# Kernel optimization log

Measured on AMD Instinct MI355X. Metric: run time of the kernel, lower is better.

Reference implementation:

```python
import jax, jax.numpy as jnp
import numpy as np
import math

HIDDEN, HEADS, D_K = 768, 12, 64
BS, SEQ = 4, 2048


def setup_inputs() -> dict:
    key = jax.random.key(0)
    ks = jax.random.split(key, 5)
    s = 1.0 / math.sqrt(HIDDEN)
    return {
        "x": jax.random.normal(ks[0], (BS, SEQ, HIDDEN), dtype=jnp.float32),
        "Wq": jax.random.normal(ks[1], (HIDDEN, HIDDEN), dtype=jnp.float32) * s,
        "bq": jnp.zeros((HIDDEN,), jnp.float32),
        "Wk": jax.random.normal(ks[2], (HIDDEN, HIDDEN), dtype=jnp.float32) * s,
        "bk": jnp.zeros((HIDDEN,), jnp.float32),
        "Wv": jax.random.normal(ks[3], (HIDDEN, HIDDEN), dtype=jnp.float32) * s,
        "bv": jnp.zeros((HIDDEN,), jnp.float32),
        "Wo": jax.random.normal(ks[4], (HIDDEN, HIDDEN), dtype=jnp.float32) * s,
        "bo": jnp.zeros((HIDDEN,), jnp.float32),
    }


def reference(x, Wq, bq, Wk, bk, Wv, bv, Wo, bo):
    bs, seq, _ = x.shape
    # projections; nn.Linear computes x @ W.T + b
    def proj(W, b):
        y = jnp.einsum("bsd,ed->bse", x, W) + b
        return y.reshape(bs, seq, HEADS, D_K).transpose(0, 2, 1, 3)  # [b,h,s,d]
    q, k, v = proj(Wq, bq), proj(Wk, bk), proj(Wv, bv)
    scores = jnp.einsum("bhqd,bhkd->bhqk", q, k) / jnp.sqrt(jnp.float32(D_K))
    attn = jax.nn.softmax(scores, axis=-1)  # dropout = 0 (eval)
    ctx = jnp.einsum("bhqk,bhkd->bhqd", attn, v)
    ctx = ctx.transpose(0, 2, 1, 3).reshape(bs, seq, HIDDEN)
    return jnp.einsum("bsd,ed->bse", ctx, Wo) + bo
```

## Files before the change

### kernel.cpp

```cpp
#include <hip/hip_runtime.h>
#include <hip/hip_bf16.h>

#define HID 768
#define NHEAD 12
#define DKH 64
#define BSZ 4
#define SEQ 2048
#define MTOT (BSZ*SEQ)
#define NBH (BSZ*NHEAD)

typedef __attribute__((ext_vector_type(8))) short   s16x8;
typedef __attribute__((ext_vector_type(8))) __bf16  bf16x8;
typedef __attribute__((ext_vector_type(4))) __bf16  bf16x4;
typedef __attribute__((ext_vector_type(4))) float   f32x4;

#define MFMA16x32(A,B,C) __builtin_amdgcn_mfma_f32_16x16x32_bf16((A),(B),(C),0,0,0)

__device__ __forceinline__ unsigned short f2bf(float f) {
  union { float f; unsigned int u; } a; a.f = f;
  return (unsigned short)((a.u + 0x7FFFu + ((a.u >> 16) & 1u)) >> 16);
}

__device__ __forceinline__ void gload_lds16(const unsigned short* g, unsigned short* l) {
  __builtin_amdgcn_global_load_lds((const __attribute__((address_space(1))) void*)g,
                                   (__attribute__((address_space(3))) void*)l, 16, 0, 0);
}

__global__ __launch_bounds__(256) void cvtall_kernel(const float* __restrict__ x,
                                                     const float* __restrict__ w0,
                                                     const float* __restrict__ w1,
                                                     const float* __restrict__ w2,
                                                     const float* __restrict__ w3,
                                                     unsigned short* __restrict__ xb,
                                                     unsigned short* __restrict__ wb) {
  const int bid = blockIdx.x;
  const float* src; unsigned short* dst; int off;
  if (bid < 6144) {
    src = x; dst = xb; off = bid * 1024;
  } else {
    const int t = bid - 6144;
    const int wi = t / 576;
    const int ro = t - wi * 576;
    src = (wi == 0) ? w0 : (wi == 1) ? w1 : (wi == 2) ? w2 : w3;
    dst = wb + (size_t)wi * HID * HID;
    off = ro * 1024;
  }
  const int i = off + threadIdx.x * 4;
  float4 v = *(const float4*)(src + i);
  ushort4 o;
  o.x = f2bf(v.x); o.y = f2bf(v.y); o.z = f2bf(v.z); o.w = f2bf(v.w);
  *(ushort4*)(dst + i) = o;
}

#define GEMM_STEP(CUR, KTN, DOPREF)                                         \
  {                                                                         \
    if (DOPREF) {                                                           \
      _Pragma("unroll")                                                     \
      for (int i = 0; i < 4; ++i) {                                         \
        const int c = wave * 4 + i;                                         \
        gload_lds16(Aptr + (size_t)(c*8 + sr) * HID + (KTN) + sc8,          \
                    As[(CUR)^1] + c*512);                                   \
      }                                                                     \
      _Pragma("unroll")                                                     \
      for (int i = 0; i < NB; ++i) {                                        \
        const int c = wave * NB + i;                                        \
        gload_lds16(Wptr + (size_t)(c*8 + sr) * HID + (KTN) + sc8,          \
                    Bs[(CUR)^1] + c*512);                                   \
      }                                                                     \
    }                                                                       \
    const char* ab = (const char*)As[CUR];                                  \
    const char* bb = (const char*)Bs[CUR];                                  \
    _Pragma("unroll")                                                       \
    for (int kk = 0; kk < 2; ++kk) {                                        \
      bf16x8 af[4], bfr[NB];                                                \
      _Pragma("unroll")                                                     \
      for (int mb = 0; mb < 4; ++mb) {                                      \
        const int r = wm + mb*16 + l16;                                     \
        af[mb] = *(const bf16x8*)(ab + r*128 + (((kk*4 + lg) ^ (l16 & 7)) << 4)); \
      }                                                                     \
      _Pragma("unroll")                                                     \
      for (int nb = 0; nb < NB; ++nb) {                                     \
        const int r = wn + nb*16 + l16;                                     \
        bfr[nb] = *(const bf16x8*)(bb + r*128 + (((kk*4 + lg) ^ (l16 & 7)) << 4)); \
      }                                                                     \
      _Pragma("unroll")                                                     \
      for (int mb = 0; mb < 4; ++mb)                                        \
        _Pragma("unroll")                                                   \
        for (int nb = 0; nb < NB; ++nb)                                     \
          acc[mb][nb] = MFMA16x32(af[mb], bfr[nb], acc[mb][nb]);            \
    }                                                                       \
    __syncthreads();                                                        \
  }

template<int MODE, int NB>
__global__ __launch_bounds__(256) void gemm_kernel(
    const unsigned short* __restrict__ A,
    const unsigned short* __restrict__ W,
    const float* __restrict__ bias0,
    const float* __restrict__ bias1,
    const float* __restrict__ bias2,
    void* __restrict__ out_raw,
    unsigned short* __restrict__ vtimg)
{
  __shared__ unsigned short As[2][128*64];
  __shared__ unsigned short Bs[2][NB*32*64];
  const int tid  = threadIdx.x;
  const int wave = tid >> 6, lane = tid & 63;
  const int l16  = lane & 15, lg = lane >> 4;
  const int f    = blockIdx.x;
  const int xcd  = f & 7, rr = f >> 3;
  const int bx   = xcd*8 + (rr & 7), by = rr >> 3;
  const int m0   = bx * 128, n0 = by * (NB*32);
  const int wm   = (wave & 1) * 64,  wn = (wave >> 1) * (NB*16);

  const f32x4 z4 = {0.f, 0.f, 0.f, 0.f};
  f32x4 acc[4][NB];
#pragma unroll
  for (int i = 0; i < 4; ++i)
#pragma unroll
    for (int j = 0; j < NB; ++j) acc[i][j] = z4;

  const int sr  = lane >> 3;
  const int sc8 = ((lane & 7) ^ sr) << 3;
  const unsigned short* Aptr = A + (size_t)m0 * HID;
  const unsigned short* Wptr = W + (size_t)n0 * HID;

#pragma unroll
  for (int i = 0; i < 4; ++i) {
    const int c = wave * 4 + i;
    gload_lds16(Aptr + (size_t)(c*8 + sr) * HID + sc8, As[0] + c*512);
  }
#pragma unroll
  for (int i = 0; i < NB; ++i) {
    const int c = wave * NB + i;
    gload_lds16(Wptr + (size_t)(c*8 + sr) * HID + sc8, Bs[0] + c*512);
  }
  __syncthreads();

#pragma unroll 1
  for (int tt = 0; tt < 6; ++tt) {
    GEMM_STEP(0, (2*tt+1)*64, true)
    GEMM_STEP(1, (2*tt+2)*64, (tt < 5))
  }

  if (MODE == 0) {
    unsigned short* out = (unsigned short*)out_raw;
    const float QSCALE = 0.18033688011112042f;
    const int which = (n0 + wn) / HID;
    if (which == 2) {
      const int e_base = n0 + wn - 2*HID;
#pragma unroll
      for (int nb = 0; nb < NB; ++nb) {
        const int e = e_base + nb*16 + l16;
        const int h = e >> 6, d = e & 63;
        const float bias = bias2[e];
#pragma unroll
        for (int mb = 0; mb < 4; ++mb) {
          const int m    = m0 + wm + mb*16 + lg*4;
          const int b    = m >> 11, s = m & (SEQ - 1);
          const int tile = s >> 6;
          const int slot = ((s & 63) >> 2) ^ l16;
          ushort4 w;
          w.x = f2bf(acc[mb][nb][0] + bias);
          w.y = f2bf(acc[mb][nb][1] + bias);
          w.z = f2bf(acc[mb][nb][2] + bias);
          w.w = f2bf(acc[mb][nb][3] + bias);
          *(ushort4*)(vtimg + ((((size_t)(b*NHEAD + h)*32 + tile)*64 + d)*64 + slot*4)) = w;
        }
      }
    } else {
      const float* bp  = (which == 0) ? bias0 : bias1;
      const float scl  = (which == 0) ? QSCALE : 1.0f;
      const int e_base = n0 + wn - which*HID;
#pragma unroll
      for (int nb = 0; nb < NB; ++nb) {
        const int e = e_base + nb*16 + l16;
        const float bias = bp[e];
        const int h = e >> 6, d = e & 63;
#pragma unroll
        for (int mb = 0; mb < 4; ++mb)
#pragma unroll
          for (int j = 0; j < 4; ++j) {
            const int m = m0 + wm + mb*16 + lg*4 + j;
            const int b = m >> 11, s = m & (SEQ - 1);
            const float v = (acc[mb][nb][j] + bias) * scl;
            out[((((size_t)which*BSZ + b)*NHEAD + h)*SEQ + s)*DKH + d] = f2bf(v);
          }
      }
    }
  } else {
    float* out = (float*)out_raw;
#pragma unroll
    for (int nb = 0; nb < NB; ++nb) {
      const int n = n0 + wn + nb*16 + l16;
      const float bias = bias0[n];
#pragma unroll
      for (int mb = 0; mb < 4; ++mb)
#pragma unroll
        for (int j = 0; j < 4; ++j) {
          const int m = m0 + wm + mb*16 + lg*4 + j;
          out[(size_t)m*HID + n] = acc[mb][nb][j] + bias;
        }
    }
  }
}

#define ATTN_STEP(CUR, DOPREF)                                              \
  {                                                                         \
    if (DOPREF) {                                                           \
      gload_lds16(kSrc0, Ks[(CUR)^1] + wave*1024);                          \
      gload_lds16(kSrc1, Ks[(CUR)^1] + wave*1024 + 512);                    \
      gload_lds16(vSrc0, Vs[(CUR)^1] + wave*1024);                          \
      gload_lds16(vSrc1, Vs[(CUR)^1] + wave*1024 + 512);                    \
      kSrc0 += 64*DKH; kSrc1 += 64*DKH; vSrc0 += 4096; vSrc1 += 4096;       \
    }                                                                       \
    const char* kb = (const char*)Ks[CUR];                                  \
    const char* vb = (const char*)Vs[CUR];                                  \
    f32x4 sc[2][4];                                                         \
    __builtin_amdgcn_s_setprio(1);                                          \
    _Pragma("unroll")                                                       \
    for (int nb = 0; nb < 4; ++nb) {                                        \
      bf16x8 kf0 = *(const bf16x8*)(kb + kbase0 + nb*2048);                 \
      bf16x8 kf1 = *(const bf16x8*)(kb + kbase1 + nb*2048);                 \
      f32x4 z0 = z4, z1 = z4;                                               \
      z0 = MFMA16x32(kf0, qf[0][0], z0);                                    \
      z0 = MFMA16x32(kf1, qf[0][1], z0);                                    \
      z1 = MFMA16x32(kf0, qf[1][0], z1);                                    \
      z1 = MFMA16x32(kf1, qf[1][1], z1);                                    \
      sc[0][nb] = z0; sc[1][nb] = z1;                                       \
    }                                                                       \
    __builtin_amdgcn_s_setprio(0);                                          \
    bf16x8 pa[2][2];                                                        \
    _Pragma("unroll")                                                       \
    for (int qa = 0; qa < 2; ++qa)                                          \
      _Pragma("unroll")                                                     \
      for (int nb = 0; nb < 4; ++nb)                                        \
        _Pragma("unroll")                                                   \
        for (int j = 0; j < 4; ++j)                                         \
          pa[qa][nb>>1][(nb&1)*4 + j] =                                     \
            (__bf16)__builtin_amdgcn_exp2f(sc[qa][nb][j]);                  \
    __builtin_amdgcn_s_setprio(1);                                          \
    csum[0] = MFMA16x32(pa[0][0], ones, csum[0]);                           \
    csum[0] = MFMA16x32(pa[0][1], ones, csum[0]);                           \
    csum[1] = MFMA16x32(pa[1][0], ones, csum[1]);                           \
    csum[1] = MFMA16x32(pa[1][1], ones, csum[1]);                           \
    _Pragma("unroll")                                                       \
    for (int db = 0; db < 4; ++db) {                                        \
      bf16x4 v00 = *(const bf16x4*)(vb + vbase0 + db*2048);                 \
      bf16x4 v01 = *(const bf16x4*)(vb + vbase1 + db*2048);                 \
      bf16x4 v10 = *(const bf16x4*)(vb + vbase2 + db*2048);                 \
      bf16x4 v11 = *(const bf16x4*)(vb + vbase3 + db*2048);                 \
      bf16x8 vf0 = __builtin_shufflevector(v00, v01, 0,1,2,3,4,5,6,7);      \
      bf16x8 vf1 = __builtin_shufflevector(v10, v11, 0,1,2,3,4,5,6,7);      \
      cacc[0][db] = MFMA16x32(pa[0][0], vf0, cacc[0][db]);                  \
      cacc[0][db] = MFMA16x32(pa[0][1], vf1, cacc[0][db]);                  \
      cacc[1][db] = MFMA16x32(pa[1][0], vf0, cacc[1][db]);                  \
      cacc[1][db] = MFMA16x32(pa[1][1], vf1, cacc[1][db]);                  \
    }                                                                       \
    __builtin_amdgcn_s_setprio(0);                                          \
    __syncthreads();                                                        \
  }

__global__ __launch_bounds__(256, 3) void attn_kernel(const unsigned short* __restrict__ qkv,
                                                      const unsigned short* __restrict__ vtimg,
                                                      unsigned short* __restrict__ ctx)
{
  __shared__ unsigned short Ks[2][64*64];
  __shared__ unsigned short Vs[2][64*64];
  const int tid  = threadIdx.x;
  const int wave = tid >> 6, lane = tid & 63;
  const int l16  = lane & 15, lg = lane >> 4;
  const int f   = blockIdx.x;
  const int xcd = f & 7, idx = f >> 3;
  const int bh  = xcd * 6 + (idx >> 4);
  const int qt  = idx & 15;
  const int b   = bh / NHEAD, h = bh - b * NHEAD;
  const int q0  = qt * 128 + wave * 32;

  const unsigned short* Qg = qkv + (size_t)bh * (SEQ*DKH);
  const unsigned short* Kg = qkv + (size_t)(NBH + bh) * (SEQ*DKH);

  const int srow  = lane >> 3;
  const int scolK = ((lane & 7) ^ srow) << 3;
  const unsigned short* kSrc0 = Kg + (size_t)(wave*16 + srow) * DKH + scolK;
  const unsigned short* kSrc1 = Kg + (size_t)(wave*16 + 8 + srow) * DKH + scolK;
  const unsigned short* vSrc0 = vtimg + ((size_t)bh*32*64 + wave*16 + srow) * 64 + (lane & 7) * 8;
  const unsigned short* vSrc1 = vSrc0 + 8*64;

  const int kbase0 = l16*128 + ((lg ^ (l16 & 7)) << 4);
  const int kbase1 = l16*128 + (((lg + 4) ^ (l16 & 7)) << 4);
  const int vbase0 = l16*128 + (((lg     ) ^ l16) << 3);
  const int vbase1 = l16*128 + (((lg +  4) ^ l16) << 3);
  const int vbase2 = l16*128 + (((lg +  8) ^ l16) << 3);
  const int vbase3 = l16*128 + (((lg + 12) ^ l16) << 3);

  bf16x8 qf[2][2];
#pragma unroll
  for (int qa = 0; qa < 2; ++qa) {
    qf[qa][0] = *(const bf16x8*)(Qg + (size_t)(q0 + qa*16 + l16)*DKH + lg*8);
    qf[qa][1] = *(const bf16x8*)(Qg + (size_t)(q0 + qa*16 + l16)*DKH + 32 + lg*8);
  }

  bf16x8 ones;
#pragma unroll
  for (int e = 0; e < 8; ++e) ones[e] = (__bf16)1.0f;

  const f32x4 z4 = {0.f,0.f,0.f,0.f};
  f32x4 cacc[2][4];
  f32x4 csum[2] = {z4, z4};
#pragma unroll
  for (int qa = 0; qa < 2; ++qa)
#pragma unroll
    for (int db = 0; db < 4; ++db) cacc[qa][db] = z4;

  gload_lds16(kSrc0, Ks[0] + wave*1024);
  gload_lds16(kSrc1, Ks[0] + wave*1024 + 512);
  gload_lds16(vSrc0, Vs[0] + wave*1024);
  gload_lds16(vSrc1, Vs[0] + wave*1024 + 512);
  kSrc0 += 64*DKH; kSrc1 += 64*DKH; vSrc0 += 4096; vSrc1 += 4096;
  __syncthreads();

#pragma unroll 1
  for (int tt = 0; tt < 16; ++tt) {
    ATTN_STEP(0, true)
    ATTN_STEP(1, (tt < 15))
  }

#pragma unroll
  for (int qa = 0; qa < 2; ++qa) {
    f32x4 inv;
#pragma unroll
    for (int j = 0; j < 4; ++j) inv[j] = 1.0f / csum[qa][j];
#pragma unroll
    for (int db = 0; db < 4; ++db)
#pragma unroll
      for (int j = 0; j < 4; ++j) {
        const int srow2 = q0 + qa*16 + lg*4 + j;
        ctx[((size_t)(b*SEQ + srow2))*HID + h*DKH + db*16 + l16] = f2bf(cacc[qa][db][j] * inv[j]);
      }
  }
}

extern "C" void kernel_launch(void* const* d_in, const int* in_sizes, int n_in,
                              void* d_out, int out_size, void* d_ws, size_t ws_size,
                              hipStream_t stream) {
  (void)in_sizes; (void)n_in; (void)out_size; (void)ws_size;
  const float* x  = (const float*)d_in[0];
  const float* Wq = (const float*)d_in[1];
  const float* bq = (const float*)d_in[2];
  const float* Wk = (const float*)d_in[3];
  const float* bk = (const float*)d_in[4];
  const float* Wv = (const float*)d_in[5];
  const float* bv = (const float*)d_in[6];
  const float* Wo = (const float*)d_in[7];
  const float* bo = (const float*)d_in[8];

  unsigned short* ws   = (unsigned short*)d_ws;
  unsigned short* Xb   = ws;
  unsigned short* Wqkv = Xb + (size_t)MTOT * HID;
  unsigned short* Wob  = Wqkv + (size_t)3 * HID * HID;
  unsigned short* qkvb = Wob + (size_t)HID * HID;
  unsigned short* vtb  = qkvb + (size_t)2 * NBH * SEQ * DKH;
  unsigned short* ctxb = Xb;

  cvtall_kernel<<<6144 + 4*576, 256, 0, stream>>>(x, Wq, Wk, Wv, Wo, Xb, Wqkv);

  gemm_kernel<0,6><<<768, 256, 0, stream>>>(Xb, Wqkv, bq, bk, bv, qkvb, vtb);
  attn_kernel<<<768, 256, 0, stream>>>(qkvb, vtb, ctxb);
  gemm_kernel<1,3><<<512, 256, 0, stream>>>(ctxb, Wob, bo, nullptr, nullptr, d_out, nullptr);
}
```

Baseline: 136.7 us.

## Use square 128x128 GEMM tiles and 128-key attention tiles

Both GEMMs now use a fixed 128x128 output tile in place of the 128x192 (QKV) and 128x96 (output projection) tiles, which changes grid sizes to 1152 and 384 blocks. The attention kernel now stages 128 keys per double-buffered LDS step, processed as two 64-key sub-steps, which halves the number of barriers and prefetch rounds. The cost is twice the LDS per attention block, with launch bounds lowered from 3 to 2 blocks per CU, so occupancy drops. The V-image indexing is reworked to match the larger tiles.

```diff
diff --git a/kernel.cpp b/kernel.cpp
--- a/kernel.cpp
+++ b/kernel.cpp
@@ -60,10 +60,6 @@
         const int c = wave * 4 + i;                                         \
         gload_lds16(Aptr + (size_t)(c*8 + sr) * HID + (KTN) + sc8,          \
                     As[(CUR)^1] + c*512);                                   \
-      }                                                                     \
-      _Pragma("unroll")                                                     \
-      for (int i = 0; i < NB; ++i) {                                        \
-        const int c = wave * NB + i;                                        \
         gload_lds16(Wptr + (size_t)(c*8 + sr) * HID + (KTN) + sc8,          \
                     Bs[(CUR)^1] + c*512);                                   \
       }                                                                     \
@@ -72,27 +68,27 @@
     const char* bb = (const char*)Bs[CUR];                                  \
     _Pragma("unroll")                                                       \
     for (int kk = 0; kk < 2; ++kk) {                                        \
-      bf16x8 af[4], bfr[NB];                                                \
+      bf16x8 af[4], bfr[4];                                                 \
       _Pragma("unroll")                                                     \
       for (int mb = 0; mb < 4; ++mb) {                                      \
         const int r = wm + mb*16 + l16;                                     \
         af[mb] = *(const bf16x8*)(ab + r*128 + (((kk*4 + lg) ^ (l16 & 7)) << 4)); \
       }                                                                     \
       _Pragma("unroll")                                                     \
-      for (int nb = 0; nb < NB; ++nb) {                                     \
+      for (int nb = 0; nb < 4; ++nb) {                                      \
         const int r = wn + nb*16 + l16;                                     \
         bfr[nb] = *(const bf16x8*)(bb + r*128 + (((kk*4 + lg) ^ (l16 & 7)) << 4)); \
       }                                                                     \
       _Pragma("unroll")                                                     \
       for (int mb = 0; mb < 4; ++mb)                                        \
         _Pragma("unroll")                                                   \
-        for (int nb = 0; nb < NB; ++nb)                                     \
+        for (int nb = 0; nb < 4; ++nb)                                      \
           acc[mb][nb] = MFMA16x32(af[mb], bfr[nb], acc[mb][nb]);            \
     }                                                                       \
     __syncthreads();                                                        \
   }
 
-template<int MODE, int NB>
+template<int MODE>
 __global__ __launch_bounds__(256) void gemm_kernel(
     const unsigned short* __restrict__ A,
     const unsigned short* __restrict__ W,
@@ -103,22 +99,22 @@
     unsigned short* __restrict__ vtimg)
 {
   __shared__ unsigned short As[2][128*64];
-  __shared__ unsigned short Bs[2][NB*32*64];
+  __shared__ unsigned short Bs[2][128*64];
   const int tid  = threadIdx.x;
   const int wave = tid >> 6, lane = tid & 63;
   const int l16  = lane & 15, lg = lane >> 4;
   const int f    = blockIdx.x;
   const int xcd  = f & 7, rr = f >> 3;
   const int bx   = xcd*8 + (rr & 7), by = rr >> 3;
-  const int m0   = bx * 128, n0 = by * (NB*32);
-  const int wm   = (wave & 1) * 64,  wn = (wave >> 1) * (NB*16);
+  const int m0   = bx * 128, n0 = by * 128;
+  const int wm   = (wave & 1) * 64,  wn = (wave >> 1) * 64;
 
   const f32x4 z4 = {0.f, 0.f, 0.f, 0.f};
-  f32x4 acc[4][NB];
+  f32x4 acc[4][4];
 #pragma unroll
   for (int i = 0; i < 4; ++i)
 #pragma unroll
-    for (int j = 0; j < NB; ++j) acc[i][j] = z4;
+    for (int j = 0; j < 4; ++j) acc[i][j] = z4;
 
   const int sr  = lane >> 3;
   const int sc8 = ((lane & 7) ^ sr) << 3;
@@ -129,10 +125,6 @@
   for (int i = 0; i < 4; ++i) {
     const int c = wave * 4 + i;
     gload_lds16(Aptr + (size_t)(c*8 + sr) * HID + sc8, As[0] + c*512);
-  }
-#pragma unroll
-  for (int i = 0; i < NB; ++i) {
-    const int c = wave * NB + i;
     gload_lds16(Wptr + (size_t)(c*8 + sr) * HID + sc8, Bs[0] + c*512);
   }
   __syncthreads();
@@ -148,12 +140,11 @@
     const float QSCALE = 0.18033688011112042f;
     const int which = (n0 + wn) / HID;
     if (which == 2) {
-      const int e_base = n0 + wn - 2*HID;
-#pragma unroll
-      for (int nb = 0; nb < NB; ++nb) {
-        const int e = e_base + nb*16 + l16;
-        const int h = e >> 6, d = e & 63;
-        const float bias = bias2[e];
+      const int h = (n0 + wn - 2*HID) >> 6;
+#pragma unroll
+      for (int nb = 0; nb < 4; ++nb) {
+        const int d = nb*16 + l16;
+        const float bias = bias2[h*64 + d];
 #pragma unroll
         for (int mb = 0; mb < 4; ++mb) {
           const int m    = m0 + wm + mb*16 + lg*4;
@@ -173,7 +164,7 @@
       const float scl  = (which == 0) ? QSCALE : 1.0f;
       const int e_base = n0 + wn - which*HID;
 #pragma unroll
-      for (int nb = 0; nb < NB; ++nb) {
+      for (int nb = 0; nb < 4; ++nb) {
         const int e = e_base + nb*16 + l16;
         const float bias = bp[e];
         const int h = e >> 6, d = e & 63;
@@ -191,7 +182,7 @@
   } else {
     float* out = (float*)out_raw;
 #pragma unroll
-    for (int nb = 0; nb < NB; ++nb) {
+    for (int nb = 0; nb < 4; ++nb) {
       const int n = n0 + wn + nb*16 + l16;
       const float bias = bias0[n];
 #pragma unroll
@@ -205,17 +196,10 @@
   }
 }
 
-#define ATTN_STEP(CUR, DOPREF)                                              \
+#define ATTN_SUB(KB, VB)                                                    \
   {                                                                         \
-    if (DOPREF) {                                                           \
-      gload_lds16(kSrc0, Ks[(CUR)^1] + wave*1024);                          \
-      gload_lds16(kSrc1, Ks[(CUR)^1] + wave*1024 + 512);                    \
-      gload_lds16(vSrc0, Vs[(CUR)^1] + wave*1024);                          \
-      gload_lds16(vSrc1, Vs[(CUR)^1] + wave*1024 + 512);                    \
-      kSrc0 += 64*DKH; kSrc1 += 64*DKH; vSrc0 += 4096; vSrc1 += 4096;       \
-    }                                                                       \
-    const char* kb = (const char*)Ks[CUR];                                  \
-    const char* vb = (const char*)Vs[CUR];                                  \
+    const char* kb = (KB);                                                  \
+    const char* vb = (VB);                                                  \
     f32x4 sc[2][4];                                                         \
     __builtin_amdgcn_s_setprio(1);                                          \
     _Pragma("unroll")                                                       \
@@ -258,15 +242,29 @@
       cacc[1][db] = MFMA16x32(pa[1][1], vf1, cacc[1][db]);                  \
     }                                                                       \
     __builtin_amdgcn_s_setprio(0);                                          \
+  }
+
+#define ATTN_STEP(CUR, DOPREF)                                              \
+  {                                                                         \
+    if (DOPREF) {                                                           \
+      _Pragma("unroll")                                                     \
+      for (int i = 0; i < 4; ++i) {                                         \
+        gload_lds16(kSrc[i], Ks[(CUR)^1] + (wave*4+i)*512);                 \
+        gload_lds16(vSrc[i], Vs[(CUR)^1] + (wave*4+i)*512);                 \
+        kSrc[i] += 128*DKH; vSrc[i] += 2*4096;                              \
+      }                                                                     \
+    }                                                                       \
+    ATTN_SUB((const char*)Ks[CUR],          (const char*)Vs[CUR])           \
+    ATTN_SUB((const char*)Ks[CUR] + 8192,   (const char*)Vs[CUR] + 8192)    \
     __syncthreads();                                                        \
   }
 
-__global__ __launch_bounds__(256, 3) void attn_kernel(const unsigned short* __restrict__ qkv,
+__global__ __launch_bounds__(256, 2) void attn_kernel(const unsigned short* __restrict__ qkv,
                                                       const unsigned short* __restrict__ vtimg,
                                                       unsigned short* __restrict__ ctx)
 {
-  __shared__ unsigned short Ks[2][64*64];
-  __shared__ unsigned short Vs[2][64*64];
+  __shared__ unsigned short Ks[2][128*64];
+  __shared__ unsigned short Vs[2][128*64];
   const int tid  = threadIdx.x;
   const int wave = tid >> 6, lane = tid & 63;
   const int l16  = lane & 15, lg = lane >> 4;
@@ -279,13 +277,17 @@
 
   const unsigned short* Qg = qkv + (size_t)bh * (SEQ*DKH);
   const unsigned short* Kg = qkv + (size_t)(NBH + bh) * (SEQ*DKH);
+  const unsigned short* Vg = vtimg + (size_t)bh * 32 * 4096;
 
   const int srow  = lane >> 3;
   const int scolK = ((lane & 7) ^ srow) << 3;
-  const unsigned short* kSrc0 = Kg + (size_t)(wave*16 + srow) * DKH + scolK;
-  const unsigned short* kSrc1 = Kg + (size_t)(wave*16 + 8 + srow) * DKH + scolK;
-  const unsigned short* vSrc0 = vtimg + ((size_t)bh*32*64 + wave*16 + srow) * 64 + (lane & 7) * 8;
-  const unsigned short* vSrc1 = vSrc0 + 8*64;
+  const unsigned short* kSrc[4];
+  const unsigned short* vSrc[4];
+#pragma unroll
+  for (int i = 0; i < 4; ++i) {
+    kSrc[i] = Kg + (size_t)(wave*32 + i*8 + srow) * DKH + scolK;
+    vSrc[i] = Vg + (wave*4 + i)*512 + lane*8;
+  }
 
   const int kbase0 = l16*128 + ((lg ^ (l16 & 7)) << 4);
   const int kbase1 = l16*128 + (((lg + 4) ^ (l16 & 7)) << 4);
@@ -313,17 +315,18 @@
 #pragma unroll
     for (int db = 0; db < 4; ++db) cacc[qa][db] = z4;
 
-  gload_lds16(kSrc0, Ks[0] + wave*1024);
-  gload_lds16(kSrc1, Ks[0] + wave*1024 + 512);
-  gload_lds16(vSrc0, Vs[0] + wave*1024);
-  gload_lds16(vSrc1, Vs[0] + wave*1024 + 512);
-  kSrc0 += 64*DKH; kSrc1 += 64*DKH; vSrc0 += 4096; vSrc1 += 4096;
+#pragma unroll
+  for (int i = 0; i < 4; ++i) {
+    gload_lds16(kSrc[i], Ks[0] + (wave*4+i)*512);
+    gload_lds16(vSrc[i], Vs[0] + (wave*4+i)*512);
+    kSrc[i] += 128*DKH; vSrc[i] += 2*4096;
+  }
   __syncthreads();
 
 #pragma unroll 1
-  for (int tt = 0; tt < 16; ++tt) {
+  for (int tt = 0; tt < 8; ++tt) {
     ATTN_STEP(0, true)
-    ATTN_STEP(1, (tt < 15))
+    ATTN_STEP(1, (tt < 7))
   }
 
 #pragma unroll
@@ -365,7 +368,7 @@
 
   cvtall_kernel<<<6144 + 4*576, 256, 0, stream>>>(x, Wq, Wk, Wv, Wo, Xb, Wqkv);
 
-  gemm_kernel<0,6><<<768, 256, 0, stream>>>(Xb, Wqkv, bq, bk, bv, qkvb, vtb);
+  gemm_kernel<0><<<1152, 256, 0, stream>>>(Xb, Wqkv, bq, bk, bv, qkvb, vtb);
   attn_kernel<<<768, 256, 0, stream>>>(qkvb, vtb, ctxb);
-  gemm_kernel<1,3><<<512, 256, 0, stream>>>(ctxb, Wob, bo, nullptr, nullptr, d_out, nullptr);
-}
+  gemm_kernel<1><<<384, 256, 0, stream>>>(ctxb, Wob, bo, nullptr, nullptr, d_out, nullptr);
+}
```

Measured after the change: 134.7 us. About the same (-1.5%).
